# Optimization experiments

Measured on AMD Instinct MI355X. Metric: run time of the kernel, lower is better.

## Reference

```python
import jax, jax.numpy as jnp
import numpy as np

B, N, D = 8, 2048, 512  # batch, input_dim (tokens), weight_dim


def setup_inputs() -> dict:
    key = jax.random.key(0)
    ks = jax.random.split(key, 7)
    return {
        "query": jax.random.normal(ks[0], (B, N, D), dtype=jnp.float32),
        "key": jax.random.normal(ks[1], (B, N, D), dtype=jnp.float32),
        "value": jax.random.normal(ks[2], (B, N, D), dtype=jnp.float32),
        "W_query": jax.random.normal(ks[3], (D, D), dtype=jnp.float32),
        "W_key": jax.random.normal(ks[4], (D, D), dtype=jnp.float32),
        "W_value": jax.random.normal(ks[5], (D, D), dtype=jnp.float32),
        "self_importance": jnp.zeros((N,), dtype=jnp.float32),
    }


def reference(query, key, value, W_query, W_key, W_value, self_importance):
    d = W_query.shape[0]
    q = jnp.einsum("bnd,de->bne", query, W_query)
    k = jnp.einsum("bnd,de->bne", key, W_key)
    v = jnp.einsum("bnd,de->bne", value, W_value)
    scores = jnp.einsum("bqe,bke->bqk", q, k) / jnp.sqrt(jnp.float32(d))
    # diagonal self-importance bias: eye(N) * clamp(exp(s), max=3)
    importance = jnp.minimum(jnp.exp(self_importance), 3.0)  # [N]
    n = scores.shape[1]
    idx = jnp.arange(n)
    scores = scores.at[:, idx, idx].add(importance)
    attn = jax.nn.softmax(scores, axis=-1)  # [B, N, N]
    entropy_loss = -jnp.mean(jnp.sum(attn * jnp.log(attn + 1e-10), axis=-1))
    out = jnp.einsum("bqk,bke->bqe", attn, v)
    return (out, attn, entropy_loss)
```

## Files before the change

### kernel.cpp

```cpp
#include <hip/hip_runtime.h>
#include <math.h>

#define BB 8
#define NN 2048
#define DD 512

typedef _Float16 halfT;
typedef _Float16 half8 __attribute__((ext_vector_type(8)));
typedef _Float16 half4 __attribute__((ext_vector_type(4)));
typedef float f32x4 __attribute__((ext_vector_type(4)));

#define GLOAD16(gp, sp) __builtin_amdgcn_global_load_lds( \
    (const __attribute__((address_space(1))) void*)(gp), \
    (__attribute__((address_space(3))) void*)(sp), 16, 0, 0)

__global__ __launch_bounds__(256) void wsplit_kernel(
    const float* __restrict__ Wq, const float* __restrict__ Wk, const float* __restrict__ Wv,
    _Float16* __restrict__ qhT, _Float16* __restrict__ qlT,
    _Float16* __restrict__ khT, _Float16* __restrict__ klT,
    _Float16* __restrict__ vhT)
{
    __shared__ float t[64][65];
    const int z = blockIdx.z;
    const float* W = (z == 0) ? Wq : ((z == 1) ? Wk : Wv);
    _Float16* Ph = (z == 0) ? qhT : ((z == 1) ? khT : vhT);
    _Float16* Pl = (z == 0) ? qlT : ((z == 1) ? klT : nullptr);
    const int bx = blockIdx.x * 64, by = blockIdx.y * 64;
    const int tid = threadIdx.x;
    #pragma unroll
    for (int i = 0; i < 16; ++i) {
        const int idx = i * 256 + tid;
        const int r = idx >> 6, c = idx & 63;
        t[r][c] = W[(long)(by + r) * 512 + bx + c];
    }
    __syncthreads();
    #pragma unroll
    for (int i = 0; i < 16; ++i) {
        const int idx = i * 256 + tid;
        const int r = idx >> 6, c = idx & 63;
        const float v = t[c][r];
        const _Float16 h = (_Float16)v;
        const long o = (long)(bx + r) * 512 + by + c;
        Ph[o] = h;
        if (z < 2) Pl[o] = (_Float16)(v - (float)h);
    }
}

__global__ __launch_bounds__(256) void projqk_kernel(
    const float* __restrict__ Af0, const float* __restrict__ Af1,
    const _Float16* __restrict__ B0h, const _Float16* __restrict__ B0l,
    const _Float16* __restrict__ B1h, const _Float16* __restrict__ B1l,
    _Float16* __restrict__ O0h, _Float16* __restrict__ O0l,
    _Float16* __restrict__ O1h, _Float16* __restrict__ O1l)
{
    __shared__ __align__(16) _Float16 smem[4 * 128 * 32];
    _Float16* Ah = smem;
    _Float16* Bh = smem + 4096;
    _Float16* Al = smem + 8192;
    _Float16* Bl = smem + 12288;

    const int z = blockIdx.z;
    const float* Af = z ? Af1 : Af0;
    const _Float16* Bgh = z ? B1h : B0h;
    const _Float16* Bgl = z ? B1l : B0l;
    _Float16* Oh = z ? O1h : O0h;
    _Float16* Ol = z ? O1l : O0l;

    const int tid  = threadIdx.x;
    const int lane = tid & 63;
    const int w    = tid >> 6;
    const int wr   = w >> 1, wc = w & 1;
    const int bm   = blockIdx.y * 128, bn = blockIdx.x * 128;

    f32x4 acc[4][4];
    #pragma unroll
    for (int i = 0; i < 4; ++i)
        #pragma unroll
        for (int j = 0; j < 4; ++j) acc[i][j] = (f32x4)0.0f;

    for (int k0 = 0; k0 < DD; k0 += 32) {
        #pragma unroll
        for (int i = 0; i < 2; ++i) {
            const int c   = i * 256 + w * 64 + lane;
            const int row = c >> 2, sl = c & 3;
            const long g  = (long)(bn + row) * DD + k0 + sl * 8;
            const int lb  = (i * 256 + w * 64) * 8;
            GLOAD16(Bgh + g, Bh + lb);
            GLOAD16(Bgl + g, Bl + lb);
        }
        #pragma unroll
        for (int i = 0; i < 4; ++i) {
            const int c = tid + i * 256;
            const int row = c >> 3, q4 = c & 7;
            const float4 v = *(const float4*)(Af + (long)(bm + row) * DD + k0 + q4 * 4);
            half4 h;
            h[0] = (_Float16)v.x; h[1] = (_Float16)v.y;
            h[2] = (_Float16)v.z; h[3] = (_Float16)v.w;
            *(half4*)&Ah[row * 32 + q4 * 4] = h;
            half4 l;
            l[0] = (_Float16)(v.x - (float)h[0]);
            l[1] = (_Float16)(v.y - (float)h[1]);
            l[2] = (_Float16)(v.z - (float)h[2]);
            l[3] = (_Float16)(v.w - (float)h[3]);
            *(half4*)&Al[row * 32 + q4 * 4] = l;
        }
        __syncthreads();

        half8 ah[4], bh[4], al[4], bl[4];
        #pragma unroll
        for (int f = 0; f < 4; ++f) {
            const int ar = wr * 64 + f * 16 + (lane & 15);
            const int ao = ar * 32 + ((lane >> 4) << 3);
            ah[f] = *(const half8*)&Ah[ao];
            al[f] = *(const half8*)&Al[ao];
            const int br = wc * 64 + f * 16 + (lane & 15);
            const int bo = br * 32 + ((lane >> 4) << 3);
            bh[f] = *(const half8*)&Bh[bo];
            bl[f] = *(const half8*)&Bl[bo];
        }
        #pragma unroll
        for (int i = 0; i < 4; ++i)
            #pragma unroll
            for (int j = 0; j < 4; ++j) {
                acc[i][j] = __builtin_amdgcn_mfma_f32_16x16x32_f16(ah[i], bh[j], acc[i][j], 0, 0, 0);
                acc[i][j] = __builtin_amdgcn_mfma_f32_16x16x32_f16(ah[i], bl[j], acc[i][j], 0, 0, 0);
                acc[i][j] = __builtin_amdgcn_mfma_f32_16x16x32_f16(al[i], bh[j], acc[i][j], 0, 0, 0);
            }
        __syncthreads();
    }

    #pragma unroll
    for (int i = 0; i < 4; ++i) {
        const int rb = bm + wr * 64 + i * 16 + ((lane >> 4) << 2);
        #pragma unroll
        for (int j = 0; j < 4; ++j) {
            const int gc = bn + wc * 64 + j * 16 + (lane & 15);
            #pragma unroll
            for (int r = 0; r < 4; ++r) {
                const float vv = acc[i][j][r];
                const _Float16 h = (_Float16)vv;
                const long o = (long)(rb + r) * DD + gc;
                Oh[o] = h;
                Ol[o] = (_Float16)(vv - (float)h);
            }
        }
    }
}

template<int EPI>
__global__ __launch_bounds__(256) void mm_nt(
    const float* __restrict__ Af,
    const _Float16* __restrict__ Agh,
    const _Float16* __restrict__ Bgh,
    float* __restrict__ Of, _Float16* __restrict__ Oh,
    int N, int K, long sAb, long sBb, long sOb)
{
    constexpr bool A_FP32 = (EPI == 1);

    __shared__ __align__(16) _Float16 smem[2 * 128 * 32];
    _Float16* Ah = smem;
    _Float16* Bh = smem + 4096;

    const int tid  = threadIdx.x;
    const int lane = tid & 63;
    const int w    = tid >> 6;
    const int wr   = w >> 1, wc = w & 1;
    const int z    = blockIdx.z;
    const int bm   = blockIdx.y * 128, bn = blockIdx.x * 128;

    const float* Afz = nullptr;
    const _Float16* Aghz = nullptr;
    if constexpr (A_FP32) { Afz = Af + (long)z * sAb; }
    else { Aghz = Agh + (long)z * sAb; }
    const _Float16* Bghz = Bgh + (long)z * sBb;

    f32x4 acc[4][4];
    #pragma unroll
    for (int i = 0; i < 4; ++i)
        #pragma unroll
        for (int j = 0; j < 4; ++j) acc[i][j] = (f32x4)0.0f;

    for (int k0 = 0; k0 < K; k0 += 32) {
        #pragma unroll
        for (int i = 0; i < 2; ++i) {
            const int c   = i * 256 + w * 64 + lane;
            const int row = c >> 2, sl = c & 3;
            const long g  = (long)(bn + row) * K + k0 + sl * 8;
            const int lb  = (i * 256 + w * 64) * 8;
            GLOAD16(Bghz + g, Bh + lb);
        }
        if constexpr (A_FP32) {
            #pragma unroll
            for (int i = 0; i < 4; ++i) {
                const int c = tid + i * 256;
                const int row = c >> 3, q4 = c & 7;
                const float4 v = *(const float4*)(Afz + (long)(bm + row) * K + k0 + q4 * 4);
                half4 h;
                h[0] = (_Float16)v.x; h[1] = (_Float16)v.y;
                h[2] = (_Float16)v.z; h[3] = (_Float16)v.w;
                *(half4*)&Ah[row * 32 + q4 * 4] = h;
            }
        } else {
            #pragma unroll
            for (int i = 0; i < 2; ++i) {
                const int c   = i * 256 + w * 64 + lane;
                const int row = c >> 2, sl = c & 3;
                const long g  = (long)(bm + row) * K + k0 + sl * 8;
                const int lb  = (i * 256 + w * 64) * 8;
                GLOAD16(Aghz + g, Ah + lb);
            }
        }
        __syncthreads();

        half8 ah[4], bh[4];
        #pragma unroll
        for (int f = 0; f < 4; ++f) {
            const int ar = wr * 64 + f * 16 + (lane & 15);
            const int ao = ar * 32 + ((lane >> 4) << 3);
            ah[f] = *(const half8*)&Ah[ao];
            const int br = wc * 64 + f * 16 + (lane & 15);
            const int bo = br * 32 + ((lane >> 4) << 3);
            bh[f] = *(const half8*)&Bh[bo];
        }
        #pragma unroll
        for (int i = 0; i < 4; ++i)
            #pragma unroll
            for (int j = 0; j < 4; ++j)
                acc[i][j] = __builtin_amdgcn_mfma_f32_16x16x32_f16(ah[i], bh[j], acc[i][j], 0, 0, 0);
        __syncthreads();
    }

    #pragma unroll
    for (int i = 0; i < 4; ++i) {
        const int rb = bm + wr * 64 + i * 16 + ((lane >> 4) << 2);
        #pragma unroll
        for (int j = 0; j < 4; ++j) {
            const int gc = bn + wc * 64 + j * 16 + (lane & 15);
            if constexpr (EPI == 1) {
                half4 hv;
                #pragma unroll
                for (int r = 0; r < 4; ++r) hv[r] = (_Float16)acc[i][j][r];
                const int b = rb >> 11, rIn = rb & 2047;
                *(half4*)&Oh[((long)b * 512 + gc) * 2048 + rIn] = hv;
            } else {
                float* O = Of + (long)z * sOb;
                #pragma unroll
                for (int r = 0; r < 4; ++r)
                    O[(long)(rb + r) * N + gc] = acc[i][j][r];
            }
        }
    }
}

__global__ __launch_bounds__(512, 2) void scores256_kernel(
    const halfT* __restrict__ qh, const halfT* __restrict__ ql,
    const halfT* __restrict__ kh, const halfT* __restrict__ kl,
    float* __restrict__ C, const float* __restrict__ si, float scale)
{
    extern __shared__ __align__(16) char smem[];

    const int tid  = threadIdx.x;
    const int lane = tid & 63;
    const int w    = tid >> 6;
    const int wr   = w >> 2, wc = w & 3;

    int flat = (blockIdx.z << 6) | (blockIdx.y << 3) | blockIdx.x;
    flat = ((flat & 7) << 6) | (flat >> 3);
    const int bx = flat & 7, by = (flat >> 3) & 7, bz = flat >> 6;
    const int bm = by * 256, bn = bx * 256;

    const long zoff = (long)bz * NN * DD;
    const halfT* A_h = qh + zoff;
    const halfT* A_l = ql + zoff;
    const halfT* B_h = kh + zoff;
    const halfT* B_l = kl + zoff;

    const int s_row   = w * 16 + (lane >> 2);
    const int s_chunk = (lane & 3) ^ ((lane >> 3) & 3);
    const long gA = (long)(bm + s_row) * DD + s_chunk * 8;
    const long gB = (long)(bn + s_row) * DD + s_chunk * 8;
    const int ldst = w * 1024;

#define STAGE_UNIT(P, G, T, S) do { \
        const long _kk = (long)(T) * 32; \
        GLOAD16((P) + (G) + _kk,                  smem + (S) * 16384 + ldst); \
        GLOAD16((P) + (G) + (long)128 * DD + _kk, smem + (S) * 16384 + 8192 + ldst); \
    } while (0)

    const int lr   = lane & 15;
    const int q16  = lane >> 4;
    const int frag = lr * 64 + ((q16 ^ ((lr >> 1) & 3)) << 4);
    const int abase = wr * 8192 + frag;
    const int bbase = wc * 4096 + frag;

    f32x4 acc[8][4];
    #pragma unroll
    for (int m = 0; m < 8; ++m)
        #pragma unroll
        for (int n = 0; n < 4; ++n) acc[m][n] = (f32x4)0.0f;

    STAGE_UNIT(A_h, gA, 0, 0); STAGE_UNIT(A_l, gA, 0, 1);
    STAGE_UNIT(B_h, gB, 0, 2); STAGE_UNIT(B_l, gB, 0, 3);
    STAGE_UNIT(A_h, gA, 1, 4); STAGE_UNIT(A_l, gA, 1, 5);
    STAGE_UNIT(B_h, gB, 1, 6); STAGE_UNIT(B_l, gB, 1, 7);
    asm volatile("s_waitcnt vmcnt(8)" ::: "memory");
    __builtin_amdgcn_s_barrier();
    __builtin_amdgcn_sched_barrier(0);

    for (int t = 0; t < 16; ++t) {
        const int base = (t & 1) * 4;
        const char* uAh = smem + (size_t)(base + 0) * 16384;
        const char* uAl = smem + (size_t)(base + 1) * 16384;
        const char* uBh = smem + (size_t)(base + 2) * 16384;
        const char* uBl = smem + (size_t)(base + 3) * 16384;
        const bool pf = (t < 14);

        half8 ah[8], bh[4], bl[4];
        #pragma unroll
        for (int n = 0; n < 4; ++n)
            bh[n] = *(const half8*)(uBh + bbase + n * 1024);
        #pragma unroll
        for (int m = 0; m < 8; ++m)
            ah[m] = *(const half8*)(uAh + abase + m * 1024);
        asm volatile("s_waitcnt lgkmcnt(0)" ::: "memory");
        __builtin_amdgcn_sched_barrier(0);
        __builtin_amdgcn_s_barrier();
        __builtin_amdgcn_sched_barrier(0);
        if (pf) { STAGE_UNIT(A_h, gA, t + 2, base + 0); STAGE_UNIT(B_h, gB, t + 2, base + 2); }
        __builtin_amdgcn_s_setprio(1);
        #pragma unroll
        for (int m = 0; m < 8; ++m)
            #pragma unroll
            for (int n = 0; n < 4; ++n)
                acc[m][n] = __builtin_amdgcn_mfma_f32_16x16x32_f16(ah[m], bh[n], acc[m][n], 0, 0, 0);
        __builtin_amdgcn_s_setprio(0);

        #pragma unroll
        for (int n = 0; n < 4; ++n)
            bl[n] = *(const half8*)(uBl + bbase + n * 1024);
        asm volatile("s_waitcnt lgkmcnt(0)" ::: "memory");
        __builtin_amdgcn_sched_barrier(0);
        __builtin_amdgcn_s_barrier();
        __builtin_amdgcn_sched_barrier(0);
        if (pf) STAGE_UNIT(B_l, gB, t + 2, base + 3);
        __builtin_amdgcn_s_setprio(1);
        #pragma unroll
        for (int m = 0; m < 8; ++m)
            #pragma unroll
            for (int n = 0; n < 4; ++n)
                acc[m][n] = __builtin_amdgcn_mfma_f32_16x16x32_f16(ah[m], bl[n], acc[m][n], 0, 0, 0);
        __builtin_amdgcn_s_setprio(0);

        half8 al[8];
        #pragma unroll
        for (int m = 0; m < 8; ++m)
            al[m] = *(const half8*)(uAl + abase + m * 1024);
        asm volatile("s_waitcnt lgkmcnt(0)" ::: "memory");
        __builtin_amdgcn_sched_barrier(0);
        __builtin_amdgcn_s_barrier();
        __builtin_amdgcn_sched_barrier(0);
        if (pf) STAGE_UNIT(A_l, gA, t + 2, base + 1);
        __builtin_amdgcn_s_setprio(1);
        #pragma unroll
        for (int m = 0; m < 8; ++m)
            #pragma unroll
            for (int n = 0; n < 4; ++n)
                acc[m][n] = __builtin_amdgcn_mfma_f32_16x16x32_f16(al[m], bh[n], acc[m][n], 0, 0, 0);
        __builtin_amdgcn_s_setprio(0);

        if (t < 15) {
            if (t < 14) { asm volatile("s_waitcnt vmcnt(8)" ::: "memory"); }
            else        { asm volatile("s_waitcnt vmcnt(0)" ::: "memory"); }
            __builtin_amdgcn_s_barrier();
            __builtin_amdgcn_sched_barrier(0);
        }
    }
#undef STAGE_UNIT

    float* Cz = C + (long)bz * NN * NN;
    #pragma unroll
    for (int m = 0; m < 8; ++m) {
        const int rb = bm + wr * 128 + m * 16 + ((lane >> 4) << 2);
        #pragma unroll
        for (int n = 0; n < 4; ++n) {
            const int gc = bn + wc * 64 + n * 16 + (lane & 15);
            #pragma unroll
            for (int r = 0; r < 4; ++r) {
                const int gr = rb + r;
                float vv = acc[m][n][r] * scale;
                if (gr == gc) vv += fminf(expf(si[gr]), 3.0f);
                Cz[(long)gr * NN + gc] = vv;
            }
        }
    }
}

__global__ __launch_bounds__(256) void softmax_entropy_kernel(
    float* __restrict__ attn, _Float16* __restrict__ ah, float* __restrict__ partials)
{
    __shared__ float red[4];
    const long row = blockIdx.x;
    float* p = attn + row * (long)NN;
    _Float16* ph = ah + row * (long)NN;
    const int tid = threadIdx.x;
    const int base = tid * 8;

    float4 va = *(const float4*)(p + base);
    float4 vb = *(const float4*)(p + base + 4);
    float v[8] = {va.x, va.y, va.z, va.w, vb.x, vb.y, vb.z, vb.w};

    float m = v[0];
    #pragma unroll
    for (int i = 1; i < 8; ++i) m = fmaxf(m, v[i]);
    #pragma unroll
    for (int o = 32; o; o >>= 1) m = fmaxf(m, __shfl_xor(m, o, 64));
    if ((tid & 63) == 0) red[tid >> 6] = m;
    __syncthreads();
    m = fmaxf(fmaxf(red[0], red[1]), fmaxf(red[2], red[3]));

    float t[8];
    float s = 0.f;
    #pragma unroll
    for (int i = 0; i < 8; ++i) { t[i] = v[i] - m; v[i] = expf(t[i]); s += v[i]; }
    #pragma unroll
    for (int o = 32; o; o >>= 1) s += __shfl_xor(s, o, 64);
    __syncthreads();
    if ((tid & 63) == 0) red[tid >> 6] = s;
    __syncthreads();
    s = red[0] + red[1] + red[2] + red[3];

    const float inv = 1.0f / s;
    const float lns = logf(s);
    float e = 0.f;
    float pv[8];
    #pragma unroll
    for (int i = 0; i < 8; ++i) {
        pv[i] = v[i] * inv;
        e = fmaf(pv[i], t[i] - lns, e);
    }
    *(float4*)(p + base)     = make_float4(pv[0], pv[1], pv[2], pv[3]);
    *(float4*)(p + base + 4) = make_float4(pv[4], pv[5], pv[6], pv[7]);
    half8 h;
    #pragma unroll
    for (int i = 0; i < 8; ++i) h[i] = (_Float16)pv[i];
    *(half8*)(ph + base) = h;

    #pragma unroll
    for (int o = 32; o; o >>= 1) e += __shfl_xor(e, o, 64);
    __syncthreads();
    if ((tid & 63) == 0) red[tid >> 6] = e;
    __syncthreads();
    if (tid == 0) partials[row] = red[0] + red[1] + red[2] + red[3];
}

__global__ __launch_bounds__(256) void ent_reduce_kernel(
    const float* __restrict__ partials, float* __restrict__ ent)
{
    __shared__ float red[4];
    float s = 0.f;
    for (int i = threadIdx.x; i < BB * NN; i += 256) s += partials[i];
    #pragma unroll
    for (int o = 32; o; o >>= 1) s += __shfl_xor(s, o, 64);
    if ((threadIdx.x & 63) == 0) red[threadIdx.x >> 6] = s;
    __syncthreads();
    if (threadIdx.x == 0)
        *ent = -(red[0] + red[1] + red[2] + red[3]) / (float)(BB * NN);
}

extern "C" void kernel_launch(void* const* d_in, const int* in_sizes, int n_in,
                              void* d_out, int out_size, void* d_ws, size_t ws_size,
                              hipStream_t stream) {
    const float* query = (const float*)d_in[0];
    const float* key   = (const float*)d_in[1];
    const float* value = (const float*)d_in[2];
    const float* Wq    = (const float*)d_in[3];
    const float* Wk    = (const float*)d_in[4];
    const float* Wv    = (const float*)d_in[5];
    const float* si    = (const float*)d_in[6];

    float* out  = (float*)d_out;
    float* attn = out + (size_t)BB * NN * DD;
    float* ent  = attn + (size_t)BB * NN * NN;

    const size_t NK = (size_t)BB * NN * DD;
    _Float16* ws16 = (_Float16*)d_ws;
    _Float16* qh = ws16;
    _Float16* ql = qh + NK;
    _Float16* kh = ql + NK;
    _Float16* kl = kh + NK;
    _Float16* vT = kl + NK;
    _Float16* WqhT = vT + NK;
    _Float16* WqlT = WqhT + DD * DD;
    _Float16* WkhT = WqlT + DD * DD;
    _Float16* WklT = WkhT + DD * DD;
    _Float16* WvhT = WklT + DD * DD;
    float* partials = (float*)(WvhT + DD * DD);
    _Float16* attn_h = ws16;

    const dim3 blk(256);
    const float inv_sqrt_d = 0.044194173824159216f;

    wsplit_kernel<<<dim3(8, 8, 3), blk, 0, stream>>>(Wq, Wk, Wv,
        WqhT, WqlT, WkhT, WklT, WvhT);

    projqk_kernel<<<dim3(4, 128, 2), blk, 0, stream>>>(
        query, key, WqhT, WqlT, WkhT, WklT, qh, ql, kh, kl);
    mm_nt<1><<<dim3(4, 128, 1), blk, 0, stream>>>(
        value, nullptr, WvhT, nullptr, vT, DD, DD, 0, 0, 0);

    scores256_kernel<<<dim3(8, 8, 8), dim3(512), 131072, stream>>>(
        qh, ql, kh, kl, attn, si, inv_sqrt_d);

    softmax_entropy_kernel<<<dim3(BB * NN), blk, 0, stream>>>(attn, attn_h, partials);
    ent_reduce_kernel<<<dim3(1), blk, 0, stream>>>(partials, ent);

    mm_nt<3><<<dim3(4, 16, BB), blk, 0, stream>>>(
        nullptr, attn_h, vT, out, nullptr, DD, NN,
        (long)NN * NN, (long)DD * NN, (long)NN * DD);
}
```

Before: 336.7 us.

## Restructure QK^T GEMM pipeline to one-stage-ahead double buffering with phased barriers

The split-fp16 score GEMM changes from a two-tile-ahead prefetch, which waited on vmcnt(8), to a simpler double buffer. Each iteration issues the loads for tile t+1 into the other buffer during the first two MFMA phases, then drains with vmcnt(0) at the end. More barriers are added around each MFMA phase, and the barrier is now placed before the lgkmcnt wait. This shortens prefetch depth and adds synchronization, which may expose global-load latency in exchange for simpler scheduling.

```diff
diff --git a/kernel.cpp b/kernel.cpp
--- a/kernel.cpp
+++ b/kernel.cpp
@@ -280,12 +280,7 @@
     const long gA = (long)(bm + s_row) * DD + s_chunk * 8;
     const long gB = (long)(bn + s_row) * DD + s_chunk * 8;
     const int ldst = w * 1024;
-
-#define STAGE_UNIT(P, G, T, S) do { \
-        const long _kk = (long)(T) * 32; \
-        GLOAD16((P) + (G) + _kk,                  smem + (S) * 16384 + ldst); \
-        GLOAD16((P) + (G) + (long)128 * DD + _kk, smem + (S) * 16384 + 8192 + ldst); \
-    } while (0)
+    const long rstep = (long)128 * DD;
 
     const int lr   = lane & 15;
     const int q16  = lane >> 4;
@@ -299,34 +294,43 @@
         #pragma unroll
         for (int n = 0; n < 4; ++n) acc[m][n] = (f32x4)0.0f;
 
-    STAGE_UNIT(A_h, gA, 0, 0); STAGE_UNIT(A_l, gA, 0, 1);
-    STAGE_UNIT(B_h, gB, 0, 2); STAGE_UNIT(B_l, gB, 0, 3);
-    STAGE_UNIT(A_h, gA, 1, 4); STAGE_UNIT(A_l, gA, 1, 5);
-    STAGE_UNIT(B_h, gB, 1, 6); STAGE_UNIT(B_l, gB, 1, 7);
-    asm volatile("s_waitcnt vmcnt(8)" ::: "memory");
+    {
+        char* b0 = smem;
+        GLOAD16(A_h + gA,         b0 + ldst);
+        GLOAD16(A_h + gA + rstep, b0 + 8192 + ldst);
+        GLOAD16(A_l + gA,         b0 + 16384 + ldst);
+        GLOAD16(A_l + gA + rstep, b0 + 16384 + 8192 + ldst);
+        GLOAD16(B_h + gB,         b0 + 32768 + ldst);
+        GLOAD16(B_h + gB + rstep, b0 + 32768 + 8192 + ldst);
+        GLOAD16(B_l + gB,         b0 + 49152 + ldst);
+        GLOAD16(B_l + gB + rstep, b0 + 49152 + 8192 + ldst);
+    }
+    asm volatile("s_waitcnt vmcnt(0)" ::: "memory");
     __builtin_amdgcn_s_barrier();
     __builtin_amdgcn_sched_barrier(0);
 
     for (int t = 0; t < 16; ++t) {
-        const int base = (t & 1) * 4;
-        const char* uAh = smem + (size_t)(base + 0) * 16384;
-        const char* uAl = smem + (size_t)(base + 1) * 16384;
-        const char* uBh = smem + (size_t)(base + 2) * 16384;
-        const char* uBl = smem + (size_t)(base + 3) * 16384;
-        const bool pf = (t < 14);
-
-        half8 ah[8], bh[4], bl[4];
+        char* cur = smem + (size_t)(t & 1) * 65536;
+        char* nxt = smem + (size_t)((t + 1) & 1) * 65536;
+        const bool pf = (t < 15);
+        const long kk = (long)(t + 1) * 32;
+
+        half8 ah[8], bh[4];
         #pragma unroll
         for (int n = 0; n < 4; ++n)
-            bh[n] = *(const half8*)(uBh + bbase + n * 1024);
+            bh[n] = *(const half8*)(cur + 32768 + bbase + n * 1024);
         #pragma unroll
         for (int m = 0; m < 8; ++m)
-            ah[m] = *(const half8*)(uAh + abase + m * 1024);
+            ah[m] = *(const half8*)(cur + abase + m * 1024);
+        if (pf) {
+            GLOAD16(A_h + gA + kk,         nxt + ldst);
+            GLOAD16(A_h + gA + rstep + kk, nxt + 8192 + ldst);
+            GLOAD16(A_l + gA + kk,         nxt + 16384 + ldst);
+            GLOAD16(A_l + gA + rstep + kk, nxt + 16384 + 8192 + ldst);
+        }
+        __builtin_amdgcn_s_barrier();
         asm volatile("s_waitcnt lgkmcnt(0)" ::: "memory");
         __builtin_amdgcn_sched_barrier(0);
-        __builtin_amdgcn_s_barrier();
-        __builtin_amdgcn_sched_barrier(0);
-        if (pf) { STAGE_UNIT(A_h, gA, t + 2, base + 0); STAGE_UNIT(B_h, gB, t + 2, base + 2); }
         __builtin_amdgcn_s_setprio(1);
         #pragma unroll
         for (int m = 0; m < 8; ++m)
@@ -334,15 +338,22 @@
             for (int n = 0; n < 4; ++n)
                 acc[m][n] = __builtin_amdgcn_mfma_f32_16x16x32_f16(ah[m], bh[n], acc[m][n], 0, 0, 0);
         __builtin_amdgcn_s_setprio(0);
-
+        __builtin_amdgcn_s_barrier();
+        __builtin_amdgcn_sched_barrier(0);
+
+        half8 bl[4];
         #pragma unroll
         for (int n = 0; n < 4; ++n)
-            bl[n] = *(const half8*)(uBl + bbase + n * 1024);
+            bl[n] = *(const half8*)(cur + 49152 + bbase + n * 1024);
+        if (pf) {
+            GLOAD16(B_h + gB + kk,         nxt + 32768 + ldst);
+            GLOAD16(B_h + gB + rstep + kk, nxt + 32768 + 8192 + ldst);
+            GLOAD16(B_l + gB + kk,         nxt + 49152 + ldst);
+            GLOAD16(B_l + gB + rstep + kk, nxt + 49152 + 8192 + ldst);
+        }
+        __builtin_amdgcn_s_barrier();
         asm volatile("s_waitcnt lgkmcnt(0)" ::: "memory");
         __builtin_amdgcn_sched_barrier(0);
-        __builtin_amdgcn_s_barrier();
-        __builtin_amdgcn_sched_barrier(0);
-        if (pf) STAGE_UNIT(B_l, gB, t + 2, base + 3);
         __builtin_amdgcn_s_setprio(1);
         #pragma unroll
         for (int m = 0; m < 8; ++m)
@@ -350,16 +361,16 @@
             for (int n = 0; n < 4; ++n)
                 acc[m][n] = __builtin_amdgcn_mfma_f32_16x16x32_f16(ah[m], bl[n], acc[m][n], 0, 0, 0);
         __builtin_amdgcn_s_setprio(0);
+        __builtin_amdgcn_s_barrier();
+        __builtin_amdgcn_sched_barrier(0);
 
         half8 al[8];
         #pragma unroll
         for (int m = 0; m < 8; ++m)
-            al[m] = *(const half8*)(uAl + abase + m * 1024);
+            al[m] = *(const half8*)(cur + 16384 + abase + m * 1024);
+        __builtin_amdgcn_s_barrier();
         asm volatile("s_waitcnt lgkmcnt(0)" ::: "memory");
         __builtin_amdgcn_sched_barrier(0);
-        __builtin_amdgcn_s_barrier();
-        __builtin_amdgcn_sched_barrier(0);
-        if (pf) STAGE_UNIT(A_l, gA, t + 2, base + 1);
         __builtin_amdgcn_s_setprio(1);
         #pragma unroll
         for (int m = 0; m < 8; ++m)
@@ -367,15 +378,10 @@
             for (int n = 0; n < 4; ++n)
                 acc[m][n] = __builtin_amdgcn_mfma_f32_16x16x32_f16(al[m], bh[n], acc[m][n], 0, 0, 0);
         __builtin_amdgcn_s_setprio(0);
-
-        if (t < 15) {
-            if (t < 14) { asm volatile("s_waitcnt vmcnt(8)" ::: "memory"); }
-            else        { asm volatile("s_waitcnt vmcnt(0)" ::: "memory"); }
-            __builtin_amdgcn_s_barrier();
-            __builtin_amdgcn_sched_barrier(0);
-        }
-    }
-#undef STAGE_UNIT
+        if (pf) { asm volatile("s_waitcnt vmcnt(0)" ::: "memory"); }
+        __builtin_amdgcn_s_barrier();
+        __builtin_amdgcn_sched_barrier(0);
+    }
 
     float* Cz = C + (long)bz * NN * NN;
     #pragma unroll
```

Measured after the change: 335.7 us. Within noise of the previous version (-0.3%).
